# Optimization experiments

Hardware: AMD Instinct MI355X
Metric: run time of the kernel (lower is better)

Reference implementation:

```python
import jax, jax.numpy as jnp
import numpy as np

N = 100000      # total nodes
E = 800000      # directed edges
DIN = 256       # input feature dim
H = 128         # hidden dim
EPS = 1e-5      # BatchNorm eps


def setup_inputs() -> dict:
    key = jax.random.key(0)
    ks = jax.random.split(key, 18)
    s = 0.05
    return {
        "x": jax.random.normal(ks[0], (N, DIN), jnp.float32),
        "src": jax.random.randint(ks[1], (E,), 0, N, dtype=jnp.int32),
        "dst": jax.random.randint(ks[2], (E,), 0, N, dtype=jnp.int32),
        "W1": jax.random.normal(ks[3], (DIN, H), jnp.float32) * s,
        "b1": jnp.zeros((H,), jnp.float32),
        "g1": jnp.ones((H,), jnp.float32),
        "be1": jnp.zeros((H,), jnp.float32),
        "W2": jax.random.normal(ks[4], (H, H), jnp.float32) * s,
        "b2": jnp.zeros((H,), jnp.float32),
        "g2": jnp.ones((H,), jnp.float32),
        "be2": jnp.zeros((H,), jnp.float32),
        "W3": jax.random.normal(ks[5], (H, H), jnp.float32) * s,
        "b3": jnp.zeros((H,), jnp.float32),
        "g3": jnp.ones((H,), jnp.float32),
        "be3": jnp.zeros((H,), jnp.float32),
        "Wf": jax.random.normal(ks[6], (H, 1), jnp.float32) * s,
        "bf": jnp.zeros((1,), jnp.float32),
    }


def _gcn_conv(h, W, b, src, dst, dis):
    # GCNConv: project, then sym-normalized aggregation over edges + self-loops
    h = h @ W                                   # [N, out]
    coef = dis[src] * dis[dst]                  # [E] edge norm weights
    agg = jax.ops.segment_sum(h[src] * coef[:, None], dst, num_segments=N)
    agg = agg + h * (dis * dis)[:, None]        # self-loop term (norm = 1/deg)
    return agg + b


def _bn_relu(h, g, be):
    # BatchNorm1d in training mode (batch stats over nodes, biased variance)
    mu = jnp.mean(h, axis=0)
    var = jnp.var(h, axis=0)
    return jax.nn.relu((h - mu) * (g / jnp.sqrt(var + EPS)) + be)


def reference(x, src, dst, W1, b1, g1, be1, W2, b2, g2, be2,
              W3, b3, g3, be3, Wf, bf):
    # degree of (A + I) counted on destination nodes, edge weight 1
    deg = jax.ops.segment_sum(jnp.ones((E,), jnp.float32), dst, num_segments=N) + 1.0
    dis = jax.lax.rsqrt(deg)                    # deg >= 1, safe

    h = _bn_relu(_gcn_conv(x, W1, b1, src, dst, dis), g1, be1)
    h = _bn_relu(_gcn_conv(h, W2, b2, src, dst, dis), g2, be2)
    h = _bn_relu(_gcn_conv(h, W3, b3, src, dst, dis), g3, be3)
    return h @ Wf + bf                          # [N, 1]
```

## Files before the change

kernel.cpp:

```cpp
#include <hip/hip_runtime.h>
#include <hip/hip_bf16.h>

typedef unsigned short ushort_t;
typedef __bf16 bf16x8 __attribute__((ext_vector_type(8)));
typedef unsigned short ushort8 __attribute__((ext_vector_type(8)));
typedef unsigned short ushort4v __attribute__((ext_vector_type(4)));
typedef float f32x4 __attribute__((ext_vector_type(4)));

#define HH 128
#define EPS 1e-5f
#define STAT_SLICES 32
#define GAS __attribute__((address_space(1)))
#define LAS __attribute__((address_space(3)))

__device__ __forceinline__ float bf2f(ushort_t u) {
    unsigned v = ((unsigned)u) << 16;
    return __builtin_bit_cast(float, v);
}
__device__ __forceinline__ ushort_t f2bf(float f) {
    unsigned u = __builtin_bit_cast(unsigned, f);
    unsigned r = (u + 0x7fffu + ((u >> 16) & 1u)) >> 16;
    return (ushort_t)r;
}
__device__ __forceinline__ float cvt(const void* p, int i, int flag) {
    return flag ? bf2f(((const ushort_t*)p)[i]) : ((const float*)p)[i];
}
__device__ __forceinline__ void dma16(const void* g, void* l) {
    __builtin_amdgcn_global_load_lds((const GAS unsigned*)g, (LAS unsigned*)l, 16, 0, 0);
}

__global__ void preK(const int* __restrict__ dst, int* __restrict__ counts, int E,
                     const void* W1, ushort_t* Wt1, const void* W2, ushort_t* Wt2,
                     const void* W3, ushort_t* Wt3,
                     const void* g1, const void* b1, const void* b2, const void* b3,
                     const void* g2, const void* g3, const void* be1, const void* be2,
                     const void* be3, const void* Wfp, const void* bfp,
                     float* __restrict__ cvec, int histB) {
    const int bid = blockIdx.x;
    const int tid = threadIdx.x;
    const int flag = (((const ushort_t*)g1)[0] == 0x3F80) ? 1 : 0;
    if (bid < histB) {
        int e = bid * 256 + tid;
        if (e < E) atomicAdd(&counts[dst[e]], 1);
    } else if (bid < histB + 256) {
        int idx = (bid - histB) * 256 + tid;
        const void* W; ushort_t* Wt; int K;
        if (idx < 32768)      { W = W1; Wt = Wt1; K = 256; }
        else if (idx < 49152) { W = W2; Wt = Wt2; K = 128; idx -= 32768; }
        else                  { W = W3; Wt = Wt3; K = 128; idx -= 49152; }
        int k = idx >> 7, nn = idx & 127;
        Wt[nn * K + k] = flag ? ((const ushort_t*)W)[idx] : f2bf(((const float*)W)[idx]);
    } else {
        int t = tid;
        if (t < 128) {
            cvec[t]        = cvt(b1, t, flag);
            cvec[128 + t]  = cvt(b2, t, flag);
            cvec[256 + t]  = cvt(b3, t, flag);
            cvec[384 + t]  = cvt(g1, t, flag);
            cvec[512 + t]  = cvt(g2, t, flag);
            cvec[640 + t]  = cvt(g3, t, flag);
            cvec[768 + t]  = cvt(be1, t, flag);
            cvec[896 + t]  = cvt(be2, t, flag);
            cvec[1024 + t] = cvt(be3, t, flag);
            cvec[1152 + t] = cvt(Wfp, t, flag);
            if (t == 0) cvec[1280] = cvt(bfp, 0, flag);
        }
    }
}

__global__ void scanAdisK(const int* __restrict__ cnt, int* __restrict__ partial,
                          float* __restrict__ dis, int n, int nbScan) {
    __shared__ int lds[256];
    const int tid = threadIdx.x;
    if ((int)blockIdx.x < nbScan) {
        int base = blockIdx.x * 2048 + tid * 8;
        int s = 0;
#pragma unroll
        for (int j = 0; j < 8; ++j) { int idx = base + j; if (idx < n) s += cnt[idx]; }
        lds[tid] = s; __syncthreads();
        for (int off = 128; off; off >>= 1) { if (tid < off) lds[tid] += lds[tid + off]; __syncthreads(); }
        if (tid == 0) partial[blockIdx.x] = lds[0];
    } else {
        int i = (blockIdx.x - nbScan) * 256 + tid;
        if (i < n) dis[i] = rsqrtf((float)cnt[i] + 1.0f);
    }
}

__device__ __forceinline__ void scanC2Dev(int* lds, const int* __restrict__ cnt,
                                          const int* __restrict__ partial,
                                          int* __restrict__ rowptr, int n, int bid, int nb) {
    const int tid = threadIdx.x;
    int pre = 0, tot = 0;
    for (int i = 0; i < nb; ++i) { int v = partial[i]; if (i < bid) pre += v; tot += v; }
    int base = bid * 2048 + tid * 8;
    int v[8]; int s = 0;
#pragma unroll
    for (int j = 0; j < 8; ++j) { int idx = base + j; v[j] = (idx < n) ? cnt[idx] : 0; s += v[j]; }
    lds[tid] = s; __syncthreads();
    for (int off = 1; off < 256; off <<= 1) {
        int x = (tid >= off) ? lds[tid - off] : 0;
        __syncthreads();
        lds[tid] += x;
        __syncthreads();
    }
    int excl = lds[tid] - s;
    int off0 = pre + excl;
#pragma unroll
    for (int j = 0; j < 8; ++j) {
        int idx = base + j;
        if (idx < n) { rowptr[idx] = off0; off0 += v[j]; }
    }
    if (bid == 0 && tid == 0) rowptr[n] = tot;
}

__global__ void scatterK(const int* __restrict__ src, const int* __restrict__ dst,
                         const int* __restrict__ rowptr, int* __restrict__ fill,
                         const float* __restrict__ dis,
                         uint2* __restrict__ erec, int E) {
    int e = blockIdx.x * 256 + threadIdx.x;
    if (e >= E) return;
    int d = dst[e], s = src[e];
    int old = atomicSub(&fill[d], 1);
    int pos = rowptr[d] + old - 1;
    float c = dis[s] * dis[d];
    uint2 r; r.x = (unsigned)s; r.y = __builtin_bit_cast(unsigned, c);
    erec[pos] = r;
}

__global__ __launch_bounds__(256) void mm1scanCK(const void* __restrict__ x,
                                                 const ushort_t* __restrict__ Wt1,
                                                 ushort_t* __restrict__ tbuf, int n,
                                                 const ushort_t* __restrict__ flagRef,
                                                 const int* __restrict__ cnt,
                                                 const int* __restrict__ partial,
                                                 int* __restrict__ rowptr, int nbScan) {
    __shared__ char smem[65536];
    const int tid = threadIdx.x;
    if ((int)blockIdx.x < nbScan) {
        scanC2Dev((int*)smem, cnt, partial, rowptr, n, blockIdx.x - 0, nbScan);
        return;
    }
    const int arm = blockIdx.x - nbScan;
    const int ch  = arm & 1;

#pragma unroll
    for (int it = 0; it < 8; ++it) {
        int idx = tid + it * 256;
        int r = idx >> 5, seg = idx & 31;
        int p = seg ^ (r & 7);
        *(uint4*)&smem[r * 512 + p * 16] = *(const uint4*)&Wt1[(size_t)(ch * 64 + r) * 256 + seg * 8];
    }
    __syncthreads();

    const int lane = tid & 63, wave = tid >> 6;
    const int m = lane & 15, q = lane >> 4;
    const int flag = (flagRef[0] == 0x3F80) ? 1 : 0;
    const int nTiles = (n + 63) >> 6;
    char* abuf = smem + 32768;

    for (int tile = (arm >> 1); tile < nTiles; tile += 256) {
        const int row0 = tile * 64 + wave * 16;
        if (flag) {
#pragma unroll
            for (int j = 0; j < 8; ++j) {
                int r = row0 + j * 2;
                if (r + 1 >= n) r = n - 2;
                const char* g = (const char*)x + (size_t)r * 512 + lane * 16;
                dma16(g, abuf + (wave * 16 + j * 2) * 512);
            }
            __builtin_amdgcn_s_waitcnt(0x0F70);
        } else {
#pragma unroll
            for (int j = 0; j < 8; ++j) {
                int r = row0 + j * 2;
                if (r + 1 >= n) r = n - 2;
                int rr = r + (lane >> 5);
                int off = (lane & 31) * 8;
                const float* p = (const float*)x + (size_t)rr * 256 + off;
                float4 f0 = *(const float4*)p, f1 = *(const float4*)(p + 4);
                ushort8 v;
                v[0] = f2bf(f0.x); v[1] = f2bf(f0.y); v[2] = f2bf(f0.z); v[3] = f2bf(f0.w);
                v[4] = f2bf(f1.x); v[5] = f2bf(f1.y); v[6] = f2bf(f1.z); v[7] = f2bf(f1.w);
                *(ushort8*)&abuf[(wave * 16 + j * 2) * 512 + lane * 16] = v;
            }
        }

        f32x4 acc[4];
#pragma unroll
        for (int t = 0; t < 4; ++t) acc[t] = (f32x4){0.f, 0.f, 0.f, 0.f};
        const char* arow = abuf + (wave * 16 + m) * 512;
#pragma unroll
        for (int s = 0; s < 8; ++s) {
            ushort8 av = *(const ushort8*)(arow + s * 64 + q * 16);
            bf16x8 nf = __builtin_bit_cast(bf16x8, av);
#pragma unroll
            for (int t = 0; t < 4; ++t) {
                int p = (s * 4 + q) ^ (m & 7);
                ushort8 wv = *(const ushort8*)&smem[(t * 16 + m) * 512 + p * 16];
                acc[t] = __builtin_amdgcn_mfma_f32_16x16x32_bf16(
                    __builtin_bit_cast(bf16x8, wv), nf, acc[t], 0, 0, 0);
            }
        }
        int node = tile * 64 + wave * 16 + m;
        if (node < n) {
            ushort_t* op = tbuf + (size_t)node * HH + ch * 64 + q * 4;
#pragma unroll
            for (int t = 0; t < 4; ++t) {
                ushort4v pk;
#pragma unroll
                for (int r = 0; r < 4; ++r) pk[r] = f2bf(acc[t][r]);
                *(ushort4v*)(op + t * 16) = pk;
            }
        }
    }
}

__global__ __launch_bounds__(256) void mmBNK(const ushort_t* __restrict__ A,
                                             const ushort_t* __restrict__ Wt,
                                             ushort_t* __restrict__ out, int n,
                                             const float* __restrict__ ssum,
                                             const float* __restrict__ ssq,
                                             const float* __restrict__ gam,
                                             const float* __restrict__ bet) {
    __shared__ char smem[50176];
    char* abuf = smem + 32768;
    float* scw = (float*)(smem + 49152);
    const int tid = threadIdx.x;

    if (tid < 128) {
        float S = 0.f, Q = 0.f;
#pragma unroll
        for (int sl = 0; sl < STAT_SLICES; ++sl) { S += ssum[sl * HH + tid]; Q += ssq[sl * HH + tid]; }
        float invn = 1.0f / (float)n;
        float mu = S * invn;
        float var = fmaxf(Q * invn - mu * mu, 0.f);
        float sc = gam[tid] * rsqrtf(var + EPS);
        scw[tid] = sc;
        scw[128 + tid] = bet[tid] - mu * sc;
    }
#pragma unroll
    for (int it = 0; it < 8; ++it) {
        int idx = tid + it * 256;
        int r = idx >> 4, seg = idx & 15;
        int p = seg ^ (r & 7);
        *(uint4*)&smem[r * 256 + p * 16] = *(const uint4*)&Wt[(size_t)r * 128 + seg * 8];
    }
    __syncthreads();

    const int lane = tid & 63, wave = tid >> 6;
    const int m = lane & 15, q = lane >> 4;
    const int nTiles = (n + 63) >> 6;

    for (int tile = blockIdx.x; tile < nTiles; tile += gridDim.x) {
        const int row0 = tile * 64 + wave * 16;
#pragma unroll
        for (int j = 0; j < 4; ++j) {
            int r = row0 + j * 4;
            if (r + 3 >= n) r = n - 4;
            const char* g = (const char*)A + (size_t)r * 256 + lane * 16;
            dma16(g, abuf + (wave * 16 + j * 4) * 256);
        }
        __builtin_amdgcn_s_waitcnt(0x0F70);

        f32x4 acc[8];
#pragma unroll
        for (int t = 0; t < 8; ++t) acc[t] = (f32x4){0.f, 0.f, 0.f, 0.f};
        const char* arow = abuf + (wave * 16 + m) * 256;
#pragma unroll
        for (int s = 0; s < 4; ++s) {
            ushort8 av = *(const ushort8*)(arow + s * 64 + q * 16);
            int kb = s * 32 + q * 8;
#pragma unroll
            for (int j = 0; j < 8; ++j)
                av[j] = f2bf(fmaxf(bf2f(av[j]) * scw[kb + j] + scw[128 + kb + j], 0.f));
            bf16x8 nf = __builtin_bit_cast(bf16x8, av);
#pragma unroll
            for (int t = 0; t < 8; ++t) {
                int p = (s * 4 + q) ^ (m & 7);
                ushort8 wv = *(const ushort8*)&smem[(t * 16 + m) * 256 + p * 16];
                acc[t] = __builtin_amdgcn_mfma_f32_16x16x32_bf16(
                    __builtin_bit_cast(bf16x8, wv), nf, acc[t], 0, 0, 0);
            }
        }
        int node = tile * 64 + wave * 16 + m;
        if (node < n) {
            ushort_t* op = out + (size_t)node * HH + q * 4;
#pragma unroll
            for (int t = 0; t < 8; ++t) {
                ushort4v pk;
#pragma unroll
                for (int r = 0; r < 4; ++r) pk[r] = f2bf(acc[t][r]);
                *(ushort4v*)(op + t * 16) = pk;
            }
        }
    }
}

__global__ __launch_bounds__(256) void aggK(const ushort_t* __restrict__ t,
                                            const uint2* __restrict__ erec,
                                            const int* __restrict__ rowptr,
                                            const float* __restrict__ dis,
                                            const float* __restrict__ bias,
                                            ushort_t* __restrict__ g,
                                            float* __restrict__ ssum, float* __restrict__ ssq,
                                            int n) {
    const int lane = threadIdx.x & 63;
    const int wave = threadIdx.x >> 6;
    const int cb = lane * 2;
    const float b0 = bias[cb], b1 = bias[cb + 1];
    float s0 = 0.f, s1 = 0.f, q0 = 0.f, q1 = 0.f;

    for (int node = blockIdx.x * 4 + wave; node < n; node += gridDim.x * 4) {
        float d = dis[node];
        float d2 = d * d;
        unsigned sv = *(const unsigned*)(t + (size_t)node * HH + cb);
        float a0 = bf2f((ushort_t)(sv & 0xffff)) * d2;
        float a1 = bf2f((ushort_t)(sv >> 16)) * d2;

        int beg = rowptr[node], end = rowptr[node + 1];
        for (int eb = beg; eb < end; eb += 64) {
            int rem = end - eb; if (rem > 64) rem = 64;
            uint2 rec = (lane < rem) ? erec[eb + lane] : (uint2){0u, 0u};
            int es = (int)rec.x;
            float ec = __builtin_bit_cast(float, rec.y);
            int rr = (rem + 7) & ~7;
            for (int j = 0; j < rr; j += 8) {
                int ii[8]; float cc[8]; unsigned ww[8];
#pragma unroll
                for (int k = 0; k < 8; ++k) {
                    ii[k] = __shfl(es, j + k);
                    cc[k] = __shfl(ec, j + k);
                }
#pragma unroll
                for (int k = 0; k < 8; ++k)
                    ww[k] = *(const unsigned*)(t + (size_t)ii[k] * HH + cb);
#pragma unroll
                for (int k = 0; k < 8; ++k) {
                    a0 += bf2f((ushort_t)(ww[k] & 0xffff)) * cc[k];
                    a1 += bf2f((ushort_t)(ww[k] >> 16)) * cc[k];
                }
            }
        }
        a0 += b0; a1 += b1;
        unsigned packed = (unsigned)f2bf(a0) | ((unsigned)f2bf(a1) << 16);
        *(unsigned*)(g + (size_t)node * HH + cb) = packed;
        s0 += a0; s1 += a1; q0 += a0 * a0; q1 += a1 * a1;
    }

    __shared__ float red[4][64][4];
    red[wave][lane][0] = s0; red[wave][lane][1] = s1;
    red[wave][lane][2] = q0; red[wave][lane][3] = q1;
    __syncthreads();
    if (wave == 0) {
        float S0 = 0, S1 = 0, Q0 = 0, Q1 = 0;
#pragma unroll
        for (int w = 0; w < 4; ++w) {
            S0 += red[w][lane][0]; S1 += red[w][lane][1];
            Q0 += red[w][lane][2]; Q1 += red[w][lane][3];
        }
        int slice = (blockIdx.x & (STAT_SLICES - 1)) * HH;
        atomicAdd(&ssum[slice + cb], S0);
        atomicAdd(&ssum[slice + cb + 1], S1);
        atomicAdd(&ssq[slice + cb], Q0);
        atomicAdd(&ssq[slice + cb + 1], Q1);
    }
}

__global__ __launch_bounds__(256) void outK(const ushort_t* __restrict__ g,
                                            const float* __restrict__ ssum,
                                            const float* __restrict__ ssq,
                                            const float* __restrict__ gam,
                                            const float* __restrict__ bet,
                                            const float* __restrict__ Wf,
                                            const float* __restrict__ bfp,
                                            void* __restrict__ outv, int n,
                                            const ushort_t* __restrict__ flagRef) {
    __shared__ float scw[256];
    const int tid = threadIdx.x;
    if (tid < 128) {
        float S = 0.f, Q = 0.f;
#pragma unroll
        for (int sl = 0; sl < STAT_SLICES; ++sl) { S += ssum[sl * HH + tid]; Q += ssq[sl * HH + tid]; }
        float invn = 1.0f / (float)n;
        float mu = S * invn;
        float var = fmaxf(Q * invn - mu * mu, 0.f);
        float sc = gam[tid] * rsqrtf(var + EPS);
        scw[tid] = sc;
        scw[128 + tid] = bet[tid] - mu * sc;
    }
    __syncthreads();

    const int lane = tid & 63;
    const int wave = tid >> 6;
    const int cb = lane * 2;
    const float w0 = Wf[cb], w1 = Wf[cb + 1];
    const float sc0 = scw[cb], sc1 = scw[cb + 1];
    const float sh0 = scw[128 + cb], sh1 = scw[128 + cb + 1];
    const float bb = bfp[0];
    const int flag = (flagRef[0] == 0x3F80) ? 1 : 0;

    for (int node = blockIdx.x * 4 + wave; node < n; node += gridDim.x * 4) {
        unsigned v = *(const unsigned*)(g + (size_t)node * HH + cb);
        float h0 = fmaxf(bf2f((ushort_t)(v & 0xffff)) * sc0 + sh0, 0.f);
        float h1 = fmaxf(bf2f((ushort_t)(v >> 16)) * sc1 + sh1, 0.f);
        float x = h0 * w0 + h1 * w1;
#pragma unroll
        for (int off = 32; off; off >>= 1) x += __shfl_down(x, off);
        if (lane == 0) {
            float r = x + bb;
            if (flag) ((ushort_t*)outv)[node] = f2bf(r);
            else      ((float*)outv)[node] = r;
        }
    }
}

extern "C" void kernel_launch(void* const* d_in, const int* in_sizes, int n_in,
                              void* d_out, int out_size, void* d_ws, size_t ws_size,
                              hipStream_t stream) {
    const int DIN = 256;
    const int N = in_sizes[0] / DIN;
    const int E = in_sizes[1];

    const void* x   = d_in[0];
    const int*  src = (const int*)d_in[1];
    const int*  dst = (const int*)d_in[2];
    const void* W1  = d_in[3];
    const void* b1  = d_in[4];
    const void* g1  = d_in[5];
    const void* be1 = d_in[6];
    const void* W2  = d_in[7];
    const void* b2  = d_in[8];
    const void* g2  = d_in[9];
    const void* be2 = d_in[10];
    const void* W3  = d_in[11];
    const void* b3  = d_in[12];
    const void* g3  = d_in[13];
    const void* be3 = d_in[14];
    const void* Wf  = d_in[15];
    const void* bfp = d_in[16];
    const ushort_t* flagRef = (const ushort_t*)g1;

    char* base = (char*)d_ws;
    size_t off = 0;
    auto carve = [&](size_t bytes) -> void* {
        void* p = base + off;
        off += (bytes + 255) & ~(size_t)255;
        return p;
    };
    int*      counts = (int*)carve((size_t)N * 4);
    float*    stats  = (float*)carve((size_t)3 * 2 * STAT_SLICES * HH * 4);
    size_t    zbytes = off;
    float*    dis    = (float*)carve((size_t)N * 4);
    int*      rowptr = (int*)carve((size_t)(N + 1) * 4);
    int*      partial= (int*)carve(256 * 4);
    uint2*    erec   = (uint2*)carve((size_t)E * 8);
    ushort_t* Wt1    = (ushort_t*)carve((size_t)128 * 256 * 2);
    ushort_t* Wt2    = (ushort_t*)carve((size_t)128 * 128 * 2);
    ushort_t* Wt3    = (ushort_t*)carve((size_t)128 * 128 * 2);
    ushort_t* tbuf   = (ushort_t*)carve((size_t)N * HH * 2);
    ushort_t* gbuf   = (ushort_t*)carve((size_t)N * HH * 2);
    float*    cvec   = (float*)carve((size_t)1281 * 4);

    float* ssum0 = stats;                         float* ssq0 = ssum0 + STAT_SLICES * HH;
    float* ssum1 = ssq0 + STAT_SLICES * HH;       float* ssq1 = ssum1 + STAT_SLICES * HH;
    float* ssum2 = ssq1 + STAT_SLICES * HH;       float* ssq2 = ssum2 + STAT_SLICES * HH;

    float* c_b1 = cvec;         float* c_b2 = cvec + 128;  float* c_b3 = cvec + 256;
    float* c_g1 = cvec + 384;   float* c_g2 = cvec + 512;  float* c_g3 = cvec + 640;
    float* c_be1 = cvec + 768;  float* c_be2 = cvec + 896; float* c_be3 = cvec + 1024;
    float* c_Wf = cvec + 1152;  float* c_bf = cvec + 1280;

    const int nbScan = (N + 2047) / 2048;
    const int histB  = (E + 255) / 256;
    const int disB   = (N + 255) / 256;
    const int aggB   = 2048;

    hipMemsetAsync(d_ws, 0, zbytes, stream);

    preK<<<histB + 256 + 1, 256, 0, stream>>>(dst, counts, E, W1, Wt1, W2, Wt2, W3, Wt3,
                                              g1, b1, b2, b3, g2, g3, be1, be2, be3, Wf, bfp,
                                              cvec, histB);
    scanAdisK<<<nbScan + disB, 256, 0, stream>>>(counts, partial, dis, N, nbScan);
    mm1scanCK<<<nbScan + 512, 256, 0, stream>>>(x, Wt1, tbuf, N, flagRef,
                                                counts, partial, rowptr, nbScan);
    scatterK<<<histB, 256, 0, stream>>>(src, dst, rowptr, counts, dis, erec, E);

    aggK<<<aggB, 256, 0, stream>>>(tbuf, erec, rowptr, dis, c_b1, gbuf, ssum0, ssq0, N);
    mmBNK<<<768, 256, 0, stream>>>(gbuf, Wt2, tbuf, N, ssum0, ssq0, c_g1, c_be1);
    aggK<<<aggB, 256, 0, stream>>>(tbuf, erec, rowptr, dis, c_b2, gbuf, ssum1, ssq1, N);
    mmBNK<<<768, 256, 0, stream>>>(gbuf, Wt3, tbuf, N, ssum1, ssq1, c_g2, c_be2);
    aggK<<<aggB, 256, 0, stream>>>(tbuf, erec, rowptr, dis, c_b3, gbuf, ssum2, ssq2, N);
    outK<<<1024, 256, 0, stream>>>(gbuf, ssum2, ssq2, c_g3, c_be3, c_Wf, c_bf, d_out, N, flagRef);
}
```

Baseline: 435.7 us.

## Split wave into two half-waves gathering 8-byte rows of alternating edges

Restructures the aggregation kernel so each half of a wave handles alternating edges, with every lane loading 4 bf16 channels (8 bytes) per neighbor instead of 2. The half-wave partial sums are combined with a cross-lane shuffle, and the stats reduction is reorganized to match. The aim is wider, fewer gather loads and more edges in flight per iteration. The cost is extra shuffles, padding waste for low-degree nodes (rounding up to 16 edges), and half the lanes sitting idle during the write-out.

```diff
diff --git a/kernel.cpp b/kernel.cpp
--- a/kernel.cpp
+++ b/kernel.cpp
@@ -306,16 +306,16 @@
                                             int n) {
     const int lane = threadIdx.x & 63;
     const int wave = threadIdx.x >> 6;
-    const int cb = lane * 2;
-    const float b0 = bias[cb], b1 = bias[cb + 1];
-    float s0 = 0.f, s1 = 0.f, q0 = 0.f, q1 = 0.f;
+    const int h = lane >> 5;
+    const int c4 = (lane & 31) * 4;
+    const float bv0 = bias[c4], bv1 = bias[c4 + 1], bv2 = bias[c4 + 2], bv3 = bias[c4 + 3];
+    float st[4] = {0.f, 0.f, 0.f, 0.f}, sq[4] = {0.f, 0.f, 0.f, 0.f};
 
     for (int node = blockIdx.x * 4 + wave; node < n; node += gridDim.x * 4) {
         float d = dis[node];
         float d2 = d * d;
-        unsigned sv = *(const unsigned*)(t + (size_t)node * HH + cb);
-        float a0 = bf2f((ushort_t)(sv & 0xffff)) * d2;
-        float a1 = bf2f((ushort_t)(sv >> 16)) * d2;
+        uint2 sv = *(const uint2*)(t + (size_t)node * HH + c4);
+        float a0 = 0.f, a1 = 0.f, a2 = 0.f, a3 = 0.f;
 
         int beg = rowptr[node], end = rowptr[node + 1];
         for (int eb = beg; eb < end; eb += 64) {
@@ -323,46 +323,60 @@
             uint2 rec = (lane < rem) ? erec[eb + lane] : (uint2){0u, 0u};
             int es = (int)rec.x;
             float ec = __builtin_bit_cast(float, rec.y);
-            int rr = (rem + 7) & ~7;
-            for (int j = 0; j < rr; j += 8) {
-                int ii[8]; float cc[8]; unsigned ww[8];
+            int rr = (rem + 15) & ~15;
+            for (int j = 0; j < rr; j += 16) {
+                int ii[8]; float cc[8]; uint2 w[8];
 #pragma unroll
                 for (int k = 0; k < 8; ++k) {
-                    ii[k] = __shfl(es, j + k);
-                    cc[k] = __shfl(ec, j + k);
+                    int e = j + 2 * k + h;
+                    ii[k] = __shfl(es, e);
+                    cc[k] = __shfl(ec, e);
                 }
 #pragma unroll
                 for (int k = 0; k < 8; ++k)
-                    ww[k] = *(const unsigned*)(t + (size_t)ii[k] * HH + cb);
+                    w[k] = *(const uint2*)(t + (size_t)ii[k] * HH + c4);
 #pragma unroll
                 for (int k = 0; k < 8; ++k) {
-                    a0 += bf2f((ushort_t)(ww[k] & 0xffff)) * cc[k];
-                    a1 += bf2f((ushort_t)(ww[k] >> 16)) * cc[k];
+                    a0 += __builtin_bit_cast(float, w[k].x << 16) * cc[k];
+                    a1 += __builtin_bit_cast(float, w[k].x & 0xffff0000u) * cc[k];
+                    a2 += __builtin_bit_cast(float, w[k].y << 16) * cc[k];
+                    a3 += __builtin_bit_cast(float, w[k].y & 0xffff0000u) * cc[k];
                 }
             }
         }
-        a0 += b0; a1 += b1;
-        unsigned packed = (unsigned)f2bf(a0) | ((unsigned)f2bf(a1) << 16);
-        *(unsigned*)(g + (size_t)node * HH + cb) = packed;
-        s0 += a0; s1 += a1; q0 += a0 * a0; q1 += a1 * a1;
-    }
-
-    __shared__ float red[4][64][4];
-    red[wave][lane][0] = s0; red[wave][lane][1] = s1;
-    red[wave][lane][2] = q0; red[wave][lane][3] = q1;
+        a0 += __shfl(a0, lane ^ 32);
+        a1 += __shfl(a1, lane ^ 32);
+        a2 += __shfl(a2, lane ^ 32);
+        a3 += __shfl(a3, lane ^ 32);
+        a0 += bf2f((ushort_t)(sv.x & 0xffff)) * d2 + bv0;
+        a1 += bf2f((ushort_t)(sv.x >> 16)) * d2 + bv1;
+        a2 += bf2f((ushort_t)(sv.y & 0xffff)) * d2 + bv2;
+        a3 += bf2f((ushort_t)(sv.y >> 16)) * d2 + bv3;
+        if (h == 0) {
+            uint2 pk;
+            pk.x = (unsigned)f2bf(a0) | ((unsigned)f2bf(a1) << 16);
+            pk.y = (unsigned)f2bf(a2) | ((unsigned)f2bf(a3) << 16);
+            *(uint2*)(g + (size_t)node * HH + c4) = pk;
+            st[0] += a0; st[1] += a1; st[2] += a2; st[3] += a3;
+            sq[0] += a0 * a0; sq[1] += a1 * a1; sq[2] += a2 * a2; sq[3] += a3 * a3;
+        }
+    }
+
+    __shared__ float red[4][32][8];
+    if (h == 0) {
+#pragma unroll
+        for (int i = 0; i < 4; ++i) { red[wave][lane & 31][i] = st[i]; red[wave][lane & 31][4 + i] = sq[i]; }
+    }
     __syncthreads();
-    if (wave == 0) {
-        float S0 = 0, S1 = 0, Q0 = 0, Q1 = 0;
-#pragma unroll
-        for (int w = 0; w < 4; ++w) {
-            S0 += red[w][lane][0]; S1 += red[w][lane][1];
-            Q0 += red[w][lane][2]; Q1 += red[w][lane][3];
-        }
+    if (threadIdx.x < 128) {
+        int ch = threadIdx.x;
+        int l = ch >> 2, i = ch & 3;
+        float S = 0.f, Q = 0.f;
+#pragma unroll
+        for (int w = 0; w < 4; ++w) { S += red[w][l][i]; Q += red[w][l][4 + i]; }
         int slice = (blockIdx.x & (STAT_SLICES - 1)) * HH;
-        atomicAdd(&ssum[slice + cb], S0);
-        atomicAdd(&ssum[slice + cb + 1], S1);
-        atomicAdd(&ssq[slice + cb], Q0);
-        atomicAdd(&ssq[slice + cb + 1], Q1);
+        atomicAdd(&ssum[slice + ch], S);
+        atomicAdd(&ssq[slice + ch], Q);
     }
 }
 
```

New measurement: 470.4 us. 1.08x slower.
